# Optimization experiments

Measured on AMD Instinct MI355X. Metric: run time of the kernel, lower is better.

## Reference

```python
import jax, jax.numpy as jnp
import numpy as np
from jax import lax

B, T, L = 64, 256, 16
WV, CV, K = 50000, 128, 12
WE, CE = 512, 64
WH, CH = 512, 128
CHH, WHH = CH // 2, WH // 2
WIN = WE + CH
START, PAD, STOP = 0, 1, 2
NEG = -10000.0


def setup_inputs():
    key = jax.random.key(0)
    ks = jax.random.split(key, 26)
    def n(k, shape, s=0.1):
        return jax.random.normal(k, shape, jnp.float32) * s
    return {
        "sentence": jax.random.randint(ks[0], (B, T), 0, WV),
        "chars": jax.random.randint(ks[1], (B, T, L), 0, CV),
        "tags": jax.random.randint(ks[2], (B, T), 0, K),
        "word_embed": n(ks[3], (WV, WE)).at[PAD].set(0.0),
        "char_embed": n(ks[4], (CV, CE)).at[PAD].set(0.0),
        "cWih_f": n(ks[5], (4 * CHH, CE)), "cWhh_f": n(ks[6], (4 * CHH, CHH)), "cb_f": n(ks[7], (4 * CHH,)),
        "cWih_b": n(ks[8], (4 * CHH, CE)), "cWhh_b": n(ks[9], (4 * CHH, CHH)), "cb_b": n(ks[10], (4 * CHH,)),
        "wWih_f": n(ks[11], (4 * WHH, WIN)), "wWhh_f": n(ks[12], (4 * WHH, WHH)), "wb_f": n(ks[13], (4 * WHH,)),
        "wWih_b": n(ks[14], (4 * WHH, WIN)), "wWhh_b": n(ks[15], (4 * WHH, WHH)), "wb_b": n(ks[16], (4 * WHH,)),
        "Wtag": n(ks[17], (K, WH)), "btag": n(ks[18], (K,)),
        "transitions": jax.random.normal(ks[19], (K, K), jnp.float32).at[START, :].set(NEG).at[:, STOP].set(NEG),
        "h0c": jax.random.normal(ks[20], (2, B * T, CHH), jnp.float32),
        "c0c": jax.random.normal(ks[21], (2, B * T, CHH), jnp.float32),
        "h0w": jax.random.normal(ks[22], (2, B, WHH), jnp.float32),
        "c0w": jax.random.normal(ks[23], (2, B, WHH), jnp.float32),
    }


def _lstm(x, h0, c0, Wih, Whh, b):
    # x: [N, S, E]; torch gate order i, f, g, o
    def step(carry, xt):
        h, c = carry
        g = xt @ Wih.T + h @ Whh.T + b
        i, f, gg, o = jnp.split(g, 4, axis=-1)
        c = jax.nn.sigmoid(f) * c + jax.nn.sigmoid(i) * jnp.tanh(gg)
        h = jax.nn.sigmoid(o) * jnp.tanh(c)
        return (h, c), h
    _, hs = lax.scan(step, (h0, c0), jnp.swapaxes(x, 0, 1))
    return jnp.swapaxes(hs, 0, 1)  # [N, S, H]


def _bilstm(x, h0, c0, Wf, Uf, bf, Wb, Ub, bb):
    fwd = _lstm(x, h0[0], c0[0], Wf, Uf, bf)
    bwd = _lstm(x[:, ::-1], h0[1], c0[1], Wb, Ub, bb)[:, ::-1]
    return jnp.concatenate([fwd, bwd], axis=-1)


def _crf_forward(feats, trans):
    # feats: [B, T, K]; vectorized log-domain forward algorithm over batch
    alpha0 = jnp.full((feats.shape[0], K), NEG, feats.dtype).at[:, START].set(0.0)
    def step(alpha, emit):
        # alpha'[b, j] = logsumexp_i(alpha[b, i] + trans[j, i] + emit[b, j])
        scores = alpha[:, None, :] + trans[None, :, :] + emit[:, :, None]
        return jax.nn.logsumexp(scores, axis=-1), None
    alpha, _ = lax.scan(step, alpha0, jnp.swapaxes(feats, 0, 1))
    return jax.nn.logsumexp(alpha + trans[STOP][None, :], axis=-1)  # [B]


def _crf_gold(feats, tags, trans):
    tags_ext = jnp.concatenate([jnp.full((tags.shape[0], 1), START, tags.dtype), tags], axis=1)
    emit = jnp.take_along_axis(feats, tags[:, :, None], axis=2)[..., 0].sum(axis=1)
    tr = trans[tags_ext[:, 1:], tags_ext[:, :-1]].sum(axis=1) + trans[STOP, tags_ext[:, -1]]
    return emit + tr  # [B]


def reference(sentence, chars, tags, word_embed, char_embed, cWih_f, cWhh_f, cb_f, cWih_b, cWhh_b, cb_b, wWih_f, wWhh_f, wb_f, wWih_b, wWhh_b, wb_b, Wtag, btag, transitions, h0c, c0c, h0w, c0w):
    # char BiLSTM over B*T char sequences, take last timestep output
    ce = char_embed[chars].reshape(B * T, L, CE)
    ch = _bilstm(ce, h0c, c0c, cWih_f, cWhh_f, cb_f, cWih_b, cWhh_b, cb_b)[:, -1, :].reshape(B, T, CH)
    we = word_embed[sentence]
    x = jnp.concatenate([ch, we], axis=-1)  # [B, T, WE+CH]
    h = _bilstm(x, h0w, c0w, wWih_f, wWhh_f, wb_f, wWih_b, wWhh_b, wb_b)  # [B, T, WH]
    feats = h @ Wtag.T + btag  # [B, T, K]
    fwd_score = _crf_forward(feats, transitions)
    gold = _crf_gold(feats, tags, transitions)
    return jnp.sum(fwd_score - gold) / B
```

## Files before the change

kernel.cpp:

```cpp
#include <hip/hip_runtime.h>

#define DEVI static __device__ __forceinline__

typedef __attribute__((ext_vector_type(4))) float f32x4;
typedef __attribute__((ext_vector_type(8))) __bf16 bf16x8;
typedef __attribute__((ext_vector_type(8))) unsigned short u16x8;
typedef __attribute__((ext_vector_type(4))) unsigned short u16x4;
typedef __attribute__((ext_vector_type(8))) int i32x8;
typedef __attribute__((ext_vector_type(4))) long l64x4;
typedef __attribute__((ext_vector_type(2))) long l64x2;

DEVI unsigned short f2bf(float f) {
  union { float f; unsigned int u; } v; v.f = f;
  unsigned int u = v.u;
  u += 0x7FFFu + ((u >> 16) & 1u);
  return (unsigned short)(u >> 16);
}
DEVI float bf2f(unsigned short s) {
  union { unsigned int u; float f; } v; v.u = ((unsigned int)s) << 16;
  return v.f;
}
DEVI float sigf(float x) {
  return __builtin_amdgcn_rcpf(1.0f + __builtin_amdgcn_exp2f(-1.44269504089f * x));
}
DEVI float tanhf_(float x) {
  return 1.0f - 2.0f * __builtin_amdgcn_rcpf(1.0f + __builtin_amdgcn_exp2f(2.88539008178f * x));
}
DEVI f32x4 mfma_bf16(bf16x8 a, bf16x8 b, f32x4 c) {
  return __builtin_amdgcn_mfma_f32_16x16x32_bf16(a, b, c, 0, 0, 0);
}
DEVI f32x4 mfma_mx(i32x8 a, i32x8 b, f32x4 c) {
  return __builtin_amdgcn_mfma_scale_f32_16x16x128_f8f6f4(
      a, b, c, 0, 0, 0, 0x7F7F7F7F, 0, 0x7F7F7F7F);
}
DEVI f32x4 mfma_mx4(i32x8 a, i32x8 b, f32x4 c) {
  return __builtin_amdgcn_mfma_scale_f32_16x16x128_f8f6f4(
      a, b, c, 0, 4, 0, 0x7F7F7F7F, 0, 0x7F7F7F7F);
}
DEVI unsigned int fp4enc(float x) {
  float f = fabsf(x);
  unsigned int m;
  if      (f <  0.25f) m = 0u;
  else if (f <  0.75f) m = 1u;
  else if (f <  1.25f) m = 2u;
  else if (f <  1.75f) m = 3u;
  else if (f <  2.5f)  m = 4u;
  else if (f <  3.5f)  m = 5u;
  else if (f <  5.0f)  m = 6u;
  else                 m = 7u;
  return m | (x < 0.0f ? 8u : 0u);
}
DEVI void lds_barrier() {
  asm volatile("s_waitcnt lgkmcnt(0)" ::: "memory");
  __builtin_amdgcn_s_barrier();
}

__global__ void k_prep(const float* wih_f, const float* wih_b,
                       const float* whh_f, const float* whh_b,
                       const int* sentence, const float* wemb,
                       unsigned short* wcat8, unsigned char* whh4,
                       unsigned char* x8, float* out) {
  int bid = blockIdx.x;
  if (bid == 0 && threadIdx.x == 0) out[0] = 0.0f;
  if (bid < 2560) {
    int i = bid * 256 + threadIdx.x;
    int e = i * 2;
    int r = e / 640, c = e - r * 640;
    const float* src = (r < 1024) ? wih_f + r * 640 : wih_b + (r - 1024) * 640;
    int p = __builtin_amdgcn_cvt_pk_fp8_f32(src[c] * 16.0f, src[c + 1] * 16.0f, 0, false);
    wcat8[i] = (unsigned short)(p & 0xFFFF);
  } else if (bid < 3584) {
    int i = (bid - 2560) * 256 + threadIdx.x;
    int d = i >> 17;
    int r = i & 131071;
    int grow = r >> 7;
    int b = r & 127;
    int kt = b >> 6, rr = b & 63, lhi = rr >> 4, ib = rr & 15;
    int i0 = 2 * ib, i1 = i0 + 1;
    int k0 = kt * 128 + (i0 >> 3) * 32 + lhi * 8 + (i0 & 7);
    int k1 = kt * 128 + (i1 >> 3) * 32 + lhi * 8 + (i1 & 7);
    const float* src = d ? whh_b : whh_f;
    unsigned n0 = fp4enc(src[grow * 256 + k0] * 16.0f);
    unsigned n1 = fp4enc(src[grow * 256 + k1] * 16.0f);
    whh4[i] = (unsigned char)(n0 | (n1 << 4));
  } else {
    int gid = (bid - 3584) * 256 + threadIdx.x;
    int row = gid >> 6;
    int c8 = (gid & 63) * 8;
    int b = row & 63, t = row >> 6;
    int sent = sentence[b * 256 + t];
    const float* src = wemb + (long)sent * 512 + c8;
    unsigned long pk = 0;
    #pragma unroll
    for (int e = 0; e < 8; e += 2) {
      int p2 = __builtin_amdgcn_cvt_pk_fp8_f32(src[e] * 16.0f, src[e + 1] * 16.0f, 0, false);
      pk |= ((unsigned long)(p2 & 0xFFFF)) << (e * 8);
    }
    *(unsigned long*)&x8[row * 640 + 128 + c8] = pk;
  }
}

DEVI bf16x8 load_wfrag(const float* Wm, int rowbase, int l15, int lhi, int ks) {
  const float* p = Wm + (rowbase + l15) * 64 + ks * 32 + lhi * 8;
  u16x8 u;
  #pragma unroll
  for (int e = 0; e < 8; ++e) u[e] = f2bf(p[e]);
  return __builtin_bit_cast(bf16x8, u);
}

__launch_bounds__(256, 1)
__global__ void k_char_lstm(const int* chars, const float* cemb,
                            const float* cWih_f, const float* cWhh_f, const float* cb_f,
                            const float* cWih_b, const float* cWhh_b, const float* cb_b,
                            const float* h0c, const float* c0c,
                            unsigned char* x8) {
  __shared__ unsigned short embT[128 * 64];
  __shared__ int charsT[16 * 64];
  __shared__ unsigned short hT[64 * 72];
  const int tid = threadIdx.x;
  const int w = tid >> 6, lane = tid & 63;
  const int l15 = lane & 15, lhi = lane >> 4;
  const int sbase = blockIdx.x * 64;

  for (int idx = tid; idx < 8192; idx += 256) embT[idx] = f2bf(cemb[idx]);
  for (int idx = tid; idx < 1024; idx += 256) {
    int s = idx >> 4, t = idx & 15;
    charsT[t * 64 + s] = chars[(sbase + s) * 16 + t];
  }
  for (int idx = tid; idx < 4096; idx += 256) {
    int s = idx >> 6, u = idx & 63;
    hT[s * 72 + u] = f2bf(h0c[(sbase + s) * 64 + u]);
  }
  bf16x8 bih[4][2], bhh[4][2];
  float bias[4];
  #pragma unroll
  for (int q = 0; q < 4; ++q) {
    bias[q] = cb_f[q * 64 + w * 16 + l15];
    #pragma unroll
    for (int ks = 0; ks < 2; ++ks) {
      bih[q][ks] = load_wfrag(cWih_f, (w + 4 * q) * 16, l15, lhi, ks);
      bhh[q][ks] = load_wfrag(cWhh_f, (w + 4 * q) * 16, l15, lhi, ks);
    }
  }
  float c_[4][4];
  #pragma unroll
  for (int mt = 0; mt < 4; ++mt)
    #pragma unroll
    for (int i = 0; i < 4; ++i)
      c_[mt][i] = c0c[(sbase + mt * 16 + lhi * 4 + i) * 64 + w * 16 + l15];
  float hfin[4][4];
  #pragma unroll
  for (int mt = 0; mt < 4; ++mt)
    #pragma unroll
    for (int i = 0; i < 4; ++i) hfin[mt][i] = 0.0f;
  __syncthreads();

  for (int t = 0; t < 16; ++t) {
    bf16x8 ax[4][2], ah[4][2];
    #pragma unroll
    for (int mt = 0; mt < 4; ++mt) {
      int cidx = charsT[t * 64 + mt * 16 + l15];
      #pragma unroll
      for (int ks = 0; ks < 2; ++ks) {
        ax[mt][ks] = __builtin_bit_cast(bf16x8, *(const u16x8*)&embT[cidx * 64 + ks * 32 + lhi * 8]);
        ah[mt][ks] = __builtin_bit_cast(bf16x8, *(const u16x8*)&hT[(mt * 16 + l15) * 72 + ks * 32 + lhi * 8]);
      }
    }
    f32x4 acc[4][4];
    #pragma unroll
    for (int mt = 0; mt < 4; ++mt)
      #pragma unroll
      for (int q = 0; q < 4; ++q) acc[mt][q] = (f32x4){0.f, 0.f, 0.f, 0.f};
    #pragma unroll
    for (int ks = 0; ks < 2; ++ks)
      #pragma unroll
      for (int mt = 0; mt < 4; ++mt)
        #pragma unroll
        for (int q = 0; q < 4; ++q) {
          acc[mt][q] = mfma_bf16(ax[mt][ks], bih[q][ks], acc[mt][q]);
          acc[mt][q] = mfma_bf16(ah[mt][ks], bhh[q][ks], acc[mt][q]);
        }
    __syncthreads();
    #pragma unroll
    for (int mt = 0; mt < 4; ++mt)
      #pragma unroll
      for (int i = 0; i < 4; ++i) {
        float gi = acc[mt][0][i] + bias[0];
        float gf = acc[mt][1][i] + bias[1];
        float gg = acc[mt][2][i] + bias[2];
        float go = acc[mt][3][i] + bias[3];
        float cn = sigf(gf) * c_[mt][i] + sigf(gi) * tanhf_(gg);
        float h = sigf(go) * tanhf_(cn);
        c_[mt][i] = cn;
        if (t == 15) hfin[mt][i] = h;
        hT[(mt * 16 + lhi * 4 + i) * 72 + w * 16 + l15] = f2bf(h);
      }
    __syncthreads();
  }
  #pragma unroll
  for (int mt = 0; mt < 4; ++mt)
    #pragma unroll
    for (int i = 0; i < 4; ++i) {
      int sg = sbase + mt * 16 + lhi * 4 + i;
      int xrow = (sg & 255) * 64 + (sg >> 8);
      int p = __builtin_amdgcn_cvt_pk_fp8_f32(hfin[mt][i] * 16.0f, 0.0f, 0, false);
      x8[xrow * 640 + w * 16 + l15] = (unsigned char)(p & 0xFF);
    }
  #pragma unroll
  for (int q = 0; q < 4; ++q) {
    bias[q] = cb_b[q * 64 + w * 16 + l15];
    #pragma unroll
    for (int ks = 0; ks < 2; ++ks) {
      bih[q][ks] = load_wfrag(cWih_b, (w + 4 * q) * 16, l15, lhi, ks);
      bhh[q][ks] = load_wfrag(cWhh_b, (w + 4 * q) * 16, l15, lhi, ks);
    }
  }
  __syncthreads();
  for (int idx = tid; idx < 4096; idx += 256) {
    int s = idx >> 6, u = idx & 63;
    hT[s * 72 + u] = f2bf(h0c[16384 * 64 + (sbase + s) * 64 + u]);
  }
  __syncthreads();
  {
    bf16x8 ax[4][2], ah[4][2];
    #pragma unroll
    for (int mt = 0; mt < 4; ++mt) {
      int cidx = charsT[15 * 64 + mt * 16 + l15];
      #pragma unroll
      for (int ks = 0; ks < 2; ++ks) {
        ax[mt][ks] = __builtin_bit_cast(bf16x8, *(const u16x8*)&embT[cidx * 64 + ks * 32 + lhi * 8]);
        ah[mt][ks] = __builtin_bit_cast(bf16x8, *(const u16x8*)&hT[(mt * 16 + l15) * 72 + ks * 32 + lhi * 8]);
      }
    }
    f32x4 acc[4][4];
    #pragma unroll
    for (int mt = 0; mt < 4; ++mt)
      #pragma unroll
      for (int q = 0; q < 4; ++q) acc[mt][q] = (f32x4){0.f, 0.f, 0.f, 0.f};
    #pragma unroll
    for (int ks = 0; ks < 2; ++ks)
      #pragma unroll
      for (int mt = 0; mt < 4; ++mt)
        #pragma unroll
        for (int q = 0; q < 4; ++q) {
          acc[mt][q] = mfma_bf16(ax[mt][ks], bih[q][ks], acc[mt][q]);
          acc[mt][q] = mfma_bf16(ah[mt][ks], bhh[q][ks], acc[mt][q]);
        }
    #pragma unroll
    for (int mt = 0; mt < 4; ++mt)
      #pragma unroll
      for (int i = 0; i < 4; ++i) {
        float cc = c0c[16384 * 64 + (sbase + mt * 16 + lhi * 4 + i) * 64 + w * 16 + l15];
        float gi = acc[mt][0][i] + bias[0];
        float gf = acc[mt][1][i] + bias[1];
        float gg = acc[mt][2][i] + bias[2];
        float go = acc[mt][3][i] + bias[3];
        float cn = sigf(gf) * cc + sigf(gi) * tanhf_(gg);
        float h = sigf(go) * tanhf_(cn);
        int sg = sbase + mt * 16 + lhi * 4 + i;
        int xrow = (sg & 255) * 64 + (sg >> 8);
        int p = __builtin_amdgcn_cvt_pk_fp8_f32(h * 16.0f, 0.0f, 0, false);
        x8[xrow * 640 + 64 + w * 16 + l15] = (unsigned char)(p & 0xFF);
      }
  }
}

__launch_bounds__(256, 2)
__global__ void k_gemm_pre(const unsigned char* x8, const unsigned char* w8,
                           const float* wb_f, const float* wb_b,
                           unsigned short* pre2) {
  __shared__ __align__(16) unsigned char ldsA[2][128 * 144];
  __shared__ __align__(16) unsigned char ldsB[2][128 * 144];
  const int tid = threadIdx.x;
  const int bm = blockIdx.x >> 4, bn = blockIdx.x & 15;
  const int m0 = bm * 128, n0 = bn * 128;
  const int lane = tid & 63, w = tid >> 6;
  const int l15 = lane & 15, lhi = lane >> 4;
  const int wm = (w & 1) * 64, wn = (w >> 1) * 64;

  u16x8 ra[4], rb[4];
  auto gload = [&](int kt) {
    #pragma unroll
    for (int i = 0; i < 4; ++i) {
      int c = i * 256 + tid;
      int row = c >> 3, cb = (c & 7) * 16;
      ra[i] = *(const u16x8*)&x8[(m0 + row) * 640 + kt * 128 + cb];
      rb[i] = *(const u16x8*)&w8[(n0 + row) * 640 + kt * 128 + cb];
    }
  };
  auto swrite = [&](int buf) {
    #pragma unroll
    for (int i = 0; i < 4; ++i) {
      int c = i * 256 + tid;
      int row = c >> 3, cb = (c & 7) * 16;
      *(u16x8*)&ldsA[buf][row * 144 + cb] = ra[i];
      *(u16x8*)&ldsB[buf][row * 144 + cb] = rb[i];
    }
  };
  f32x4 acc[4][4];
  #pragma unroll
  for (int a = 0; a < 4; ++a)
    #pragma unroll
    for (int bb = 0; bb < 4; ++bb) acc[a][bb] = (f32x4){0.f, 0.f, 0.f, 0.f};

  gload(0); swrite(0); __syncthreads();
  for (int kt = 0; kt < 5; ++kt) {
    int cur = kt & 1;
    if (kt < 4) gload(kt + 1);
    i32x8 af[4], bfv[4];
    #pragma unroll
    for (int mt = 0; mt < 4; ++mt)
      af[mt] = __builtin_bit_cast(i32x8,
          *(const l64x4*)&ldsA[cur][(wm + mt * 16 + l15) * 144 + lhi * 32]);
    #pragma unroll
    for (int nt = 0; nt < 4; ++nt)
      bfv[nt] = __builtin_bit_cast(i32x8,
          *(const l64x4*)&ldsB[cur][(wn + nt * 16 + l15) * 144 + lhi * 32]);
    #pragma unroll
    for (int mt = 0; mt < 4; ++mt)
      #pragma unroll
      for (int nt = 0; nt < 4; ++nt)
        acc[mt][nt] = mfma_mx(af[mt], bfv[nt], acc[mt][nt]);
    __syncthreads();
    if (kt < 4) { swrite(cur ^ 1); __syncthreads(); }
  }
  const float inv = 1.0f / 256.0f;
  #pragma unroll
  for (int nt = 0; nt < 4; ++nt) {
    int col = n0 + wn + nt * 16 + l15;
    float bias = (col < 1024) ? wb_f[col] : wb_b[col - 1024];
    #pragma unroll
    for (int mt = 0; mt < 4; ++mt) {
      int row = m0 + wm + mt * 16 + lhi * 4;
      int t = row >> 6, b = row & 63, rg = b >> 3, b8 = b & 7;
      u16x4 v;
      #pragma unroll
      for (int i = 0; i < 4; ++i) v[i] = f2bf(acc[mt][nt][i] * inv + bias);
      *(u16x4*)&pre2[((long)(rg * 256 + t) * 2048 + col) * 8 + b8] = v;
    }
  }
}

#define LSTM_STEP(SRC, DST, PU, TT)                                          \
  {                                                                          \
    long a8[8];                                                              \
    _Pragma("unroll")                                                        \
    for (int ks = 0; ks < 8; ++ks)                                           \
      a8[ks] = *(const long*)&SRC[l15 * 264 + ks * 32 + lhi * 8];            \
    l64x4 alo4 = {a8[0], a8[1], a8[2], a8[3]};                               \
    l64x4 ahi4 = {a8[4], a8[5], a8[6], a8[7]};                               \
    i32x8 aLo = __builtin_bit_cast(i32x8, alo4);                             \
    i32x8 aHi = __builtin_bit_cast(i32x8, ahi4);                             \
    f32x4 accA[4], accB[4];                                                  \
    _Pragma("unroll")                                                        \
    for (int g = 0; g < 4; ++g) {                                            \
      accA[g] = mfma_mx4(aLo, bfr4[g][0], (f32x4){0.f, 0.f, 0.f, 0.f});      \
      accB[g] = mfma_mx4(aHi, bfr4[g][1], (f32x4){0.f, 0.f, 0.f, 0.f});      \
    }                                                                        \
    float gi = fmaf(accA[0][0] + accB[0][0], inv, bf2f(PU[0]));              \
    float gf = fmaf(accA[1][0] + accB[1][0], inv, bf2f(PU[1]));              \
    float gg = fmaf(accA[2][0] + accB[2][0], inv, bf2f(PU[2]));              \
    float go = fmaf(accA[3][0] + accB[3][0], inv, bf2f(PU[3]));              \
    float cn = sigf(gf) * c1 + sigf(gi) * tanhf_(gg);                        \
    float h = sigf(go) * tanhf_(cn);                                         \
    c1 = cn;                                                                 \
    int p2 = __builtin_amdgcn_cvt_pk_fp8_f32(h * 16.0f, 0.0f, 0, false);     \
    DST[(4 * lhi) * 264 + uu] = (unsigned char)(p2 & 0xFF);                  \
    hout[((long)(TT) * 64 + row0 + lhi) * 512 + dco] = f2bf(h);              \
  }

__launch_bounds__(1024, 4)
__global__ void k_word_lstm(const unsigned char* whh4, const unsigned short* pre2,
                            const float* h0w, const float* c0w,
                            unsigned short* hout, float* cstate, int t0) {
  __shared__ __align__(16) unsigned char hlds[2][16 * 264];
  const int tid = threadIdx.x;
  const int w = tid >> 6, lane = tid & 63;
  const int l15 = lane & 15, lhi = lane >> 4;
  const int dir = blockIdx.x >> 4, rg = blockIdx.x & 15;
  const int row0 = rg * 4;
  const int uu = w * 16 + l15;
  const int dco = dir * 256 + uu;
  const bool first = (t0 == 0);
  const unsigned char* W4 = whh4 + dir * 131072;

  i32x8 bfr4[4][2];
  #pragma unroll
  for (int g = 0; g < 4; ++g) {
    int grow = g * 256 + uu;
    #pragma unroll
    for (int kt = 0; kt < 2; ++kt) {
      l64x2 v2 = *(const l64x2*)(W4 + grow * 128 + kt * 64 + lhi * 16);
      l64x4 v = {v2[0], v2[1], 0, 0};
      bfr4[g][kt] = __builtin_bit_cast(i32x8, v);
    }
  }
  for (int idx = tid; idx < 2112; idx += 1024)
    ((unsigned int*)&hlds[0][0])[idx] = 0;
  __syncthreads();
  {
    int r = tid >> 8, u0 = tid & 255;
    float hv;
    if (first) {
      hv = h0w[dir * 16384 + (row0 + r) * 256 + u0];
    } else {
      int tb = dir ? (256 - t0) : (t0 - 1);
      hv = bf2f(hout[((long)tb * 64 + row0 + r) * 512 + dir * 256 + u0]);
    }
    int p = __builtin_amdgcn_cvt_pk_fp8_f32(hv * 16.0f, 0.0f, 0, false);
    hlds[0][(4 * r) * 264 + u0] = (unsigned char)(p & 0xFF);
  }
  float c1 = first ? c0w[dir * 16384 + (row0 + lhi) * 256 + uu]
                   : cstate[blockIdx.x * 1024 + tid];

  const unsigned short* pgBase =
      pre2 + (long)(rg >> 1) * 256 * 2048 * 8 + (dir * 1024 + uu) * 8 + (rg & 1) * 4 + lhi;

  unsigned short pA[4], pB[4];
  const int ttA0 = dir ? (255 - t0) : t0;
  #pragma unroll
  for (int g = 0; g < 4; ++g)
    pA[g] = pgBase[(long)ttA0 * 16384 + g * 2048];
  __syncthreads();

  const float inv = 1.0f / 256.0f;
  for (int tl = 0; tl < 64; tl += 2) {
    const int tg = t0 + tl;
    const int ttA = dir ? (255 - tg) : tg;
    const int ttB = dir ? (254 - tg) : (tg + 1);
    int ttC = dir ? (253 - tg) : (tg + 2);
    ttC = ttC < 0 ? 0 : (ttC > 255 ? 255 : ttC);
    #pragma unroll
    for (int g = 0; g < 4; ++g)
      pB[g] = pgBase[(long)ttB * 16384 + g * 2048];
    LSTM_STEP(hlds[0], hlds[1], pA, ttA)
    lds_barrier();
    #pragma unroll
    for (int g = 0; g < 4; ++g)
      pA[g] = pgBase[(long)ttC * 16384 + g * 2048];
    LSTM_STEP(hlds[1], hlds[0], pB, ttB)
    lds_barrier();
  }
  cstate[blockIdx.x * 1024 + tid] = c1;
}

__launch_bounds__(256, 2)
__global__ void k_feats(const unsigned short* hbuf, const float* Wtag, const float* btag,
                        float* feats) {
  const int tid = threadIdx.x;
  const int w = tid >> 6, lane = tid & 63, l15 = lane & 15, lhi = lane >> 4;
  const int m0 = blockIdx.x * 64 + w * 16;
  bf16x8 bfr[16];
  #pragma unroll
  for (int ks = 0; ks < 16; ++ks) {
    u16x8 u;
    if (l15 < 12) {
      const float* p = Wtag + l15 * 512 + ks * 32 + lhi * 8;
      #pragma unroll
      for (int e = 0; e < 8; ++e) u[e] = f2bf(p[e]);
    } else {
      #pragma unroll
      for (int e = 0; e < 8; ++e) u[e] = 0;
    }
    bfr[ks] = __builtin_bit_cast(bf16x8, u);
  }
  f32x4 acc = {0.f, 0.f, 0.f, 0.f};
  #pragma unroll
  for (int ks = 0; ks < 16; ++ks) {
    u16x8 a = *(const u16x8*)&hbuf[(m0 + l15) * 512 + ks * 32 + lhi * 8];
    acc = mfma_bf16(__builtin_bit_cast(bf16x8, a), bfr[ks], acc);
  }
  float bias = (l15 < 12) ? btag[l15] : 0.0f;
  #pragma unroll
  for (int i = 0; i < 4; ++i)
    feats[(m0 + lhi * 4 + i) * 16 + l15] = acc[i] + bias;
}

__launch_bounds__(64, 1)
__global__ void k_crf(const float* feats, const float* trans, const int* tags, float* out) {
  const int lane = threadIdx.x;
  const int lb = lane >> 4, j = lane & 15;
  const int bb = blockIdx.x * 4 + lb;
  const bool act = (j < 12);
  const int bbase = lane & 48;
  const float LOG2E = 1.44269504089f, LN2 = 0.69314718056f;

  float E[12];
  #pragma unroll
  for (int i = 0; i < 12; ++i)
    E[i] = act ? __builtin_amdgcn_exp2f(LOG2E * trans[j * 12 + i]) : 0.0f;

  float alpha = (j == 0) ? 0.0f : -10000.0f;
  const float* fp = feats + bb * 16 + j;
  float fv0 = act ? fp[0] : 0.0f;
  float fv1 = act ? fp[1024] : 0.0f;
  for (int t = 0; t < 256; ++t) {
    float fnext = act ? fp[(t + 2) * 1024] : 0.0f;
    float M = alpha;
    M = fmaxf(M, __shfl_xor(M, 1, 64));
    M = fmaxf(M, __shfl_xor(M, 2, 64));
    M = fmaxf(M, __shfl_xor(M, 4, 64));
    M = fmaxf(M, __shfl_xor(M, 8, 64));
    float e = __builtin_amdgcn_exp2f(LOG2E * (alpha - M));
    float dot = 0.0f;
    #pragma unroll
    for (int i = 0; i < 12; ++i) {
      float ei = __shfl(e, bbase + i, 64);
      dot = fmaf(E[i], ei, dot);
    }
    float nxt = fv0 + M + LN2 * __builtin_amdgcn_logf(dot);
    alpha = act ? nxt : -10000.0f;
    fv0 = fv1; fv1 = fnext;
  }
  float v = act ? (alpha + trans[2 * 12 + j]) : -3.0e38f;
  float m2 = v;
  m2 = fmaxf(m2, __shfl_xor(m2, 1, 64));
  m2 = fmaxf(m2, __shfl_xor(m2, 2, 64));
  m2 = fmaxf(m2, __shfl_xor(m2, 4, 64));
  m2 = fmaxf(m2, __shfl_xor(m2, 8, 64));
  float s = __builtin_amdgcn_exp2f(LOG2E * (v - m2));
  s += __shfl_xor(s, 1, 64);
  s += __shfl_xor(s, 2, 64);
  s += __shfl_xor(s, 4, 64);
  s += __shfl_xor(s, 8, 64);
  float part = (j == 0) ? (m2 + LN2 * __builtin_amdgcn_logf(s)) : 0.0f;
  #pragma unroll 4
  for (int k = 0; k < 16; ++k) {
    int idx = lane + 64 * k;
    int t = idx >> 2, lb2 = idx & 3;
    int b2 = blockIdx.x * 4 + lb2;
    int tg = tags[b2 * 256 + t];
    int pv = (t == 0) ? 0 : tags[b2 * 256 + t - 1];
    float g = feats[t * 1024 + b2 * 16 + tg] + trans[tg * 12 + pv];
    if (t == 255) g += trans[2 * 12 + tg];
    part -= g;
  }
  #pragma unroll
  for (int d = 1; d < 64; d <<= 1) part += __shfl_xor(part, d, 64);
  if (lane == 0) atomicAdd(out, part / 64.0f);
}

extern "C" void kernel_launch(void* const* d_in, const int* in_sizes, int n_in,
                              void* d_out, int out_size, void* d_ws, size_t ws_size,
                              hipStream_t stream) {
  const int*   sentence = (const int*)d_in[0];
  const int*   chars    = (const int*)d_in[1];
  const int*   tags     = (const int*)d_in[2];
  const float* wemb     = (const float*)d_in[3];
  const float* cemb     = (const float*)d_in[4];
  const float* cWih_f   = (const float*)d_in[5];
  const float* cWhh_f   = (const float*)d_in[6];
  const float* cb_f     = (const float*)d_in[7];
  const float* cWih_b   = (const float*)d_in[8];
  const float* cWhh_b   = (const float*)d_in[9];
  const float* cb_b     = (const float*)d_in[10];
  const float* wWih_f   = (const float*)d_in[11];
  const float* wWhh_f   = (const float*)d_in[12];
  const float* wb_f     = (const float*)d_in[13];
  const float* wWih_b   = (const float*)d_in[14];
  const float* wWhh_b   = (const float*)d_in[15];
  const float* wb_b     = (const float*)d_in[16];
  const float* Wtag     = (const float*)d_in[17];
  const float* btag     = (const float*)d_in[18];
  const float* trans    = (const float*)d_in[19];
  const float* h0c      = (const float*)d_in[20];
  const float* c0c      = (const float*)d_in[21];
  const float* h0w      = (const float*)d_in[22];
  const float* c0w      = (const float*)d_in[23];

  char* ws = (char*)d_ws;
  unsigned char*  x8    = (unsigned char*)(ws);
  unsigned short* pre2  = (unsigned short*)(ws + 20971520);
  unsigned short* hbuf  = (unsigned short*)(ws + 88080384);
  float*          feats = (float*)(ws + 104857600);
  unsigned short* wcat8 = (unsigned short*)(ws + 105906176);
  unsigned char*  whh4  = (unsigned char*)(ws + 108527616);
  float*          cstate= (float*)(ws + 108789760);

  hipLaunchKernelGGL(k_prep, dim3(7680), dim3(256), 0, stream,
                     wWih_f, wWih_b, wWhh_f, wWhh_b, sentence, wemb, wcat8, whh4, x8,
                     (float*)d_out);
  hipLaunchKernelGGL(k_char_lstm, dim3(256), dim3(256), 0, stream, chars, cemb,
                     cWih_f, cWhh_f, cb_f, cWih_b, cWhh_b, cb_b, h0c, c0c, x8);
  hipLaunchKernelGGL(k_gemm_pre, dim3(2048), dim3(256), 0, stream,
                     x8, (const unsigned char*)wcat8, wb_f, wb_b, pre2);
  hipLaunchKernelGGL(k_word_lstm, dim3(32), dim3(1024), 0, stream,
                     whh4, pre2, h0w, c0w, hbuf, cstate, 0);
  hipLaunchKernelGGL(k_word_lstm, dim3(32), dim3(1024), 0, stream,
                     whh4, pre2, h0w, c0w, hbuf, cstate, 64);
  hipLaunchKernelGGL(k_word_lstm, dim3(32), dim3(1024), 0, stream,
                     whh4, pre2, h0w, c0w, hbuf, cstate, 128);
  hipLaunchKernelGGL(k_word_lstm, dim3(32), dim3(1024), 0, stream,
                     whh4, pre2, h0w, c0w, hbuf, cstate, 192);
  hipLaunchKernelGGL(k_feats, dim3(256), dim3(256), 0, stream, hbuf, Wtag, btag, feats);
  hipLaunchKernelGGL(k_crf, dim3(16), dim3(64), 0, stream, feats, trans, tags, (float*)d_out);
}
```

Measured before the change: 468.0 us.

## Halve word-LSTM launches and run CRF one batch per lane in a single block

Result: slower. 487.9 us (+4.2%).

```diff
diff --git a/kernel.cpp b/kernel.cpp
--- a/kernel.cpp
+++ b/kernel.cpp
@@ -59,9 +59,8 @@
                        const float* whh_f, const float* whh_b,
                        const int* sentence, const float* wemb,
                        unsigned short* wcat8, unsigned char* whh4,
-                       unsigned char* x8, float* out) {
+                       unsigned char* x8) {
   int bid = blockIdx.x;
-  if (bid == 0 && threadIdx.x == 0) out[0] = 0.0f;
   if (bid < 2560) {
     int i = bid * 256 + threadIdx.x;
     int e = i * 2;
@@ -424,7 +423,7 @@
   __syncthreads();
 
   const float inv = 1.0f / 256.0f;
-  for (int tl = 0; tl < 64; tl += 2) {
+  for (int tl = 0; tl < 128; tl += 2) {
     const int tg = t0 + tl;
     const int ttA = dir ? (255 - tg) : tg;
     const int ttB = dir ? (254 - tg) : (tg + 1);
@@ -479,65 +478,71 @@
 __launch_bounds__(64, 1)
 __global__ void k_crf(const float* feats, const float* trans, const int* tags, float* out) {
   const int lane = threadIdx.x;
-  const int lb = lane >> 4, j = lane & 15;
-  const int bb = blockIdx.x * 4 + lb;
-  const bool act = (j < 12);
-  const int bbase = lane & 48;
   const float LOG2E = 1.44269504089f, LN2 = 0.69314718056f;
-
-  float E[12];
-  #pragma unroll
-  for (int i = 0; i < 12; ++i)
-    E[i] = act ? __builtin_amdgcn_exp2f(LOG2E * trans[j * 12 + i]) : 0.0f;
-
-  float alpha = (j == 0) ? 0.0f : -10000.0f;
-  const float* fp = feats + bb * 16 + j;
-  float fv0 = act ? fp[0] : 0.0f;
-  float fv1 = act ? fp[1024] : 0.0f;
+  float E[12][12], tr2[12];
+  #pragma unroll
+  for (int j = 0; j < 12; ++j) {
+    #pragma unroll
+    for (int i = 0; i < 12; ++i)
+      E[j][i] = __builtin_amdgcn_exp2f(LOG2E * trans[j * 12 + i]);
+    tr2[j] = trans[2 * 12 + j];
+  }
+  float alpha[12];
+  alpha[0] = 0.0f;
+  #pragma unroll
+  for (int j = 1; j < 12; ++j) alpha[j] = -10000.0f;
+  const float* fp = feats + lane * 16;
+  f32x4 c0 = *(const f32x4*)(fp);
+  f32x4 c1 = *(const f32x4*)(fp + 4);
+  f32x4 c2 = *(const f32x4*)(fp + 8);
   for (int t = 0; t < 256; ++t) {
-    float fnext = act ? fp[(t + 2) * 1024] : 0.0f;
-    float M = alpha;
-    M = fmaxf(M, __shfl_xor(M, 1, 64));
-    M = fmaxf(M, __shfl_xor(M, 2, 64));
-    M = fmaxf(M, __shfl_xor(M, 4, 64));
-    M = fmaxf(M, __shfl_xor(M, 8, 64));
-    float e = __builtin_amdgcn_exp2f(LOG2E * (alpha - M));
-    float dot = 0.0f;
-    #pragma unroll
-    for (int i = 0; i < 12; ++i) {
-      float ei = __shfl(e, bbase + i, 64);
-      dot = fmaf(E[i], ei, dot);
-    }
-    float nxt = fv0 + M + LN2 * __builtin_amdgcn_logf(dot);
-    alpha = act ? nxt : -10000.0f;
-    fv0 = fv1; fv1 = fnext;
-  }
-  float v = act ? (alpha + trans[2 * 12 + j]) : -3.0e38f;
-  float m2 = v;
-  m2 = fmaxf(m2, __shfl_xor(m2, 1, 64));
-  m2 = fmaxf(m2, __shfl_xor(m2, 2, 64));
-  m2 = fmaxf(m2, __shfl_xor(m2, 4, 64));
-  m2 = fmaxf(m2, __shfl_xor(m2, 8, 64));
-  float s = __builtin_amdgcn_exp2f(LOG2E * (v - m2));
-  s += __shfl_xor(s, 1, 64);
-  s += __shfl_xor(s, 2, 64);
-  s += __shfl_xor(s, 4, 64);
-  s += __shfl_xor(s, 8, 64);
-  float part = (j == 0) ? (m2 + LN2 * __builtin_amdgcn_logf(s)) : 0.0f;
-  #pragma unroll 4
-  for (int k = 0; k < 16; ++k) {
-    int idx = lane + 64 * k;
-    int t = idx >> 2, lb2 = idx & 3;
-    int b2 = blockIdx.x * 4 + lb2;
-    int tg = tags[b2 * 256 + t];
-    int pv = (t == 0) ? 0 : tags[b2 * 256 + t - 1];
-    float g = feats[t * 1024 + b2 * 16 + tg] + trans[tg * 12 + pv];
-    if (t == 255) g += trans[2 * 12 + tg];
-    part -= g;
-  }
+    const float* np = fp + (long)(t + 1) * 1024;
+    f32x4 n0 = *(const f32x4*)(np);
+    f32x4 n1 = *(const f32x4*)(np + 4);
+    f32x4 n2 = *(const f32x4*)(np + 8);
+    float M = fmaxf(fmaxf(
+        fmaxf(fmaxf(alpha[0], alpha[1]), fmaxf(alpha[2], alpha[3])),
+        fmaxf(fmaxf(alpha[4], alpha[5]), fmaxf(alpha[6], alpha[7]))),
+        fmaxf(fmaxf(alpha[8], alpha[9]), fmaxf(alpha[10], alpha[11])));
+    float e[12];
+    #pragma unroll
+    for (int i = 0; i < 12; ++i)
+      e[i] = __builtin_amdgcn_exp2f(LOG2E * (alpha[i] - M));
+    float emit[12] = {c0[0], c0[1], c0[2], c0[3],
+                      c1[0], c1[1], c1[2], c1[3],
+                      c2[0], c2[1], c2[2], c2[3]};
+    #pragma unroll
+    for (int j = 0; j < 12; ++j) {
+      float dot = 0.0f;
+      #pragma unroll
+      for (int i = 0; i < 12; ++i) dot = fmaf(E[j][i], e[i], dot);
+      alpha[j] = emit[j] + M + LN2 * __builtin_amdgcn_logf(dot);
+    }
+    c0 = n0; c1 = n1; c2 = n2;
+  }
+  float v[12];
+  #pragma unroll
+  for (int j = 0; j < 12; ++j) v[j] = alpha[j] + tr2[j];
+  float M2 = fmaxf(fmaxf(
+      fmaxf(fmaxf(v[0], v[1]), fmaxf(v[2], v[3])),
+      fmaxf(fmaxf(v[4], v[5]), fmaxf(v[6], v[7]))),
+      fmaxf(fmaxf(v[8], v[9]), fmaxf(v[10], v[11])));
+  float s = 0.0f;
+  #pragma unroll
+  for (int j = 0; j < 12; ++j)
+    s += __builtin_amdgcn_exp2f(LOG2E * (v[j] - M2));
+  float part = M2 + LN2 * __builtin_amdgcn_logf(s);
+  const int* tp = tags + lane * 256;
+  int prev = 0;
+  for (int t = 0; t < 256; ++t) {
+    int tg = tp[t];
+    part -= feats[t * 1024 + lane * 16 + tg] + trans[tg * 12 + prev];
+    prev = tg;
+  }
+  part -= trans[2 * 12 + prev];
   #pragma unroll
   for (int d = 1; d < 64; d <<= 1) part += __shfl_xor(part, d, 64);
-  if (lane == 0) atomicAdd(out, part / 64.0f);
+  if (lane == 0) out[0] = part / 64.0f;
 }
 
 extern "C" void kernel_launch(void* const* d_in, const int* in_sizes, int n_in,
@@ -578,8 +583,7 @@
   float*          cstate= (float*)(ws + 108789760);
 
   hipLaunchKernelGGL(k_prep, dim3(7680), dim3(256), 0, stream,
-                     wWih_f, wWih_b, wWhh_f, wWhh_b, sentence, wemb, wcat8, whh4, x8,
-                     (float*)d_out);
+                     wWih_f, wWih_b, wWhh_f, wWhh_b, sentence, wemb, wcat8, whh4, x8);
   hipLaunchKernelGGL(k_char_lstm, dim3(256), dim3(256), 0, stream, chars, cemb,
                      cWih_f, cWhh_f, cb_f, cWih_b, cWhh_b, cb_b, h0c, c0c, x8);
   hipLaunchKernelGGL(k_gemm_pre, dim3(2048), dim3(256), 0, stream,
@@ -587,11 +591,7 @@
   hipLaunchKernelGGL(k_word_lstm, dim3(32), dim3(1024), 0, stream,
                      whh4, pre2, h0w, c0w, hbuf, cstate, 0);
   hipLaunchKernelGGL(k_word_lstm, dim3(32), dim3(1024), 0, stream,
-                     whh4, pre2, h0w, c0w, hbuf, cstate, 64);
-  hipLaunchKernelGGL(k_word_lstm, dim3(32), dim3(1024), 0, stream,
                      whh4, pre2, h0w, c0w, hbuf, cstate, 128);
-  hipLaunchKernelGGL(k_word_lstm, dim3(32), dim3(1024), 0, stream,
-                     whh4, pre2, h0w, c0w, hbuf, cstate, 192);
   hipLaunchKernelGGL(k_feats, dim3(256), dim3(256), 0, stream, hbuf, Wtag, btag, feats);
-  hipLaunchKernelGGL(k_crf, dim3(16), dim3(64), 0, stream, feats, trans, tags, (float*)d_out);
-}
+  hipLaunchKernelGGL(k_crf, dim3(1), dim3(64), 0, stream, feats, trans, tags, (float*)d_out);
+}
```
